# Optimization experiments

Measured on AMD Instinct MI355X. Metric: run time of the kernel, lower is better.

Reference implementation:

```python
import jax, jax.numpy as jnp
import numpy as np

B, T = 64, 512
V, D, H = 50000, 256, 256  # vocab, word-embed dim, LSTM hidden


def _lstm_dir(x, Wih, Whh, bih, bhh):
    """Unidirectional LSTM over time (PyTorch gate order i,f,g,o). x: [B,T,D_in] -> [B,T,H]."""
    xp = jnp.einsum('btd,gd->btg', x, Wih) + bih + bhh  # precompute input projections [B,T,4H]
    xp = xp.transpose(1, 0, 2)  # [T,B,4H]
    Hh = Whh.shape[1]
    h0 = jnp.zeros((x.shape[0], Hh), x.dtype)

    def step(carry, xt):
        h, c = carry
        g = xt + h @ Whh.T
        i, f, gg, o = jnp.split(g, 4, axis=-1)
        c = jax.nn.sigmoid(f) * c + jax.nn.sigmoid(i) * jnp.tanh(gg)
        h = jax.nn.sigmoid(o) * jnp.tanh(c)
        return (h, c), h

    _, hs = jax.lax.scan(step, (h0, h0), xp)
    return hs.transpose(1, 0, 2)  # [B,T,H]


def _bidir(x, rev_idx, pf, pb):
    """Length-aware bidirectional layer: reverse only the valid prefix (emulates pack_padded_sequence)."""
    hf = _lstm_dir(x, *pf)
    xr = jnp.take_along_axis(x, rev_idx[..., None], axis=1)   # reversed valid prefix
    hb = _lstm_dir(xr, *pb)
    hb = jnp.take_along_axis(hb, rev_idx[..., None], axis=1)  # flip back (involution on valid part)
    return jnp.concatenate([hf, hb], axis=-1)  # [B,T,2H]


def setup_inputs() -> dict:
    key = jax.random.key(0)
    ks = jax.random.split(key, 24)
    x = jax.random.randint(ks[0], (B, T), 0, V - 1)          # avoid padding_idx = V-1
    sentlen = jax.random.randint(ks[1], (B,), 1, T + 1)       # ragged lengths in [1, T]
    embed = (jax.random.normal(ks[2], (V, D), jnp.float32) * 0.1).at[V - 1].set(0.0)
    inp = {"x": x, "sentlen": sentlen, "embed": embed}
    k = 3
    for layer, in_dim in [(0, D), (1, 2 * H)]:
        for d in ["f", "b"]:
            s = 1.0 / np.sqrt(H)
            inp[f"Wih{layer}{d}"] = jax.random.uniform(ks[k], (4 * H, in_dim), jnp.float32, -s, s); k += 1
            inp[f"Whh{layer}{d}"] = jax.random.uniform(ks[k], (4 * H, H), jnp.float32, -s, s); k += 1
            inp[f"bih{layer}{d}"] = jax.random.uniform(ks[k], (4 * H,), jnp.float32, -s, s); k += 1
            inp[f"bhh{layer}{d}"] = jax.random.uniform(ks[k], (4 * H,), jnp.float32, -s, s); k += 1
    return inp


def reference(x, sentlen, embed,
              Wih0f, Whh0f, bih0f, bhh0f, Wih0b, Whh0b, bih0b, bhh0b,
              Wih1f, Whh1f, bih1f, bhh1f, Wih1b, Whh1b, bih1b, bhh1b):
    emb = embed[x]  # [B,T,D]; dropout is a no-op in eval mode
    t = jnp.arange(x.shape[1])
    valid = t[None, :] < sentlen[:, None]                       # [B,T]
    rev_idx = jnp.where(valid, sentlen[:, None] - 1 - t[None, :], t[None, :])
    h1 = _bidir(emb, rev_idx, (Wih0f, Whh0f, bih0f, bhh0f), (Wih0b, Whh0b, bih0b, bhh0b))
    h2 = _bidir(h1, rev_idx, (Wih1f, Whh1f, bih1f, bhh1f), (Wih1b, Whh1b, bih1b, bhh1b))
    # ragged max-pool over valid positions (replaces the per-sample Python loop)
    feat = jnp.max(jnp.where(valid[..., None], h2, -jnp.inf), axis=1)  # [B,2H]
    return feat[None]  # [1,B,2H]
```

## Files before the change

### kernel.cpp

```cpp
#include <hip/hip_runtime.h>
#include <stdint.h>
#include <stddef.h>

#define BATCH 64
#define TT    512
#define DIM   256
#define HID   256
#define MROWS (BATCH*TT)

typedef unsigned short u16;
typedef unsigned int u32;
typedef __attribute__((ext_vector_type(8))) short  short8;
typedef __attribute__((ext_vector_type(4))) float  f32x4;
typedef __attribute__((ext_vector_type(4))) int    int4v;
typedef __attribute__((ext_vector_type(4))) unsigned short u16x4;

__device__ __forceinline__ u16 bf16_hi(float f) {
    union { float f; unsigned u; } v; v.f = f;
    unsigned r = v.u + 0x7fffu + ((v.u >> 16) & 1u);
    return (u16)(r >> 16);
}
__device__ __forceinline__ float bf16f(u16 b) {
    union { unsigned u; float f; } v; v.u = ((unsigned)b) << 16;
    return v.f;
}
__device__ __forceinline__ float fsigmoid(float x) { return 1.f / (1.f + __expf(-x)); }
__device__ __forceinline__ float ftanh(float x) {
    x = fminf(15.f, fmaxf(-15.f, x));
    float e = __expf(2.f * x);
    return (e - 1.f) / (e + 1.f);
}

__global__ __launch_bounds__(256) void k_prep(
    const float* __restrict__ Wih0f, const float* __restrict__ Whh0f, const float* __restrict__ bih0f, const float* __restrict__ bhh0f,
    const float* __restrict__ Wih0b, const float* __restrict__ Whh0b, const float* __restrict__ bih0b, const float* __restrict__ bhh0b,
    const float* __restrict__ Wih1f, const float* __restrict__ Whh1f, const float* __restrict__ bih1f, const float* __restrict__ bhh1f,
    const float* __restrict__ Wih1b, const float* __restrict__ Whh1b, const float* __restrict__ bih1b, const float* __restrict__ bhh1b,
    u16* __restrict__ WihQ0hi, u16* __restrict__ WihQ0lo,
    u16* __restrict__ WhhQ0hi, u16* __restrict__ WhhQ0lo,
    u16* __restrict__ WihQ1hi, u16* __restrict__ WihQ1lo,
    u16* __restrict__ WhhQ1hi, u16* __restrict__ WhhQ1lo,
    float* __restrict__ bsum, u32* __restrict__ hxp)
{
    const int i = blockIdx.x * 256 + threadIdx.x;
    if (i < 2621440) {
        const float* src; u16* dhi; u16* dlo; int off;
        if      (i <  262144) { src = Wih0f; dhi = WihQ0hi;          dlo = WihQ0lo;          off = i; }
        else if (i <  524288) { src = Wih0b; dhi = WihQ0hi + 262144; dlo = WihQ0lo + 262144; off = i -  262144; }
        else if (i <  786432) { src = Whh0f; dhi = WhhQ0hi;          dlo = WhhQ0lo;          off = i -  524288; }
        else if (i < 1048576) { src = Whh0b; dhi = WhhQ0hi + 262144; dlo = WhhQ0lo + 262144; off = i -  786432; }
        else if (i < 1572864) { src = Wih1f; dhi = WihQ1hi;          dlo = WihQ1lo;          off = i - 1048576; }
        else if (i < 2097152) { src = Wih1b; dhi = WihQ1hi + 524288; dlo = WihQ1lo + 524288; off = i - 1572864; }
        else if (i < 2359296) { src = Whh1f; dhi = WhhQ1hi;          dlo = WhhQ1lo;          off = i - 2097152; }
        else                  { src = Whh1b; dhi = WhhQ1hi + 262144; dlo = WhhQ1lo + 262144; off = i - 2359296; }
        const float v = src[off];
        const u16 h = bf16_hi(v);
        dhi[off] = h;
        dlo[off] = bf16_hi(v - bf16f(h));
    } else if (i < 2621440 + 4096) {
        const int j = i - 2621440;
        const float* bihs[4] = { bih0f, bih0b, bih1f, bih1b };
        const float* bhhs[4] = { bhh0f, bhh0b, bhh1f, bhh1b };
        const int ld = j >> 10, k = j & 1023;
        bsum[j] = bihs[ld][k] + bhhs[ld][k];
    } else if (i < 2621440 + 4096 + 131072) {
        const int j = i - (2621440 + 4096);
        hxp[j] = ((j >> 15) & 1) ? 0x00010000u : 0u;
    }
}

__global__ __launch_bounds__(256) void k_gather(
    const int* __restrict__ x, const float* __restrict__ embed, u16* __restrict__ A0)
{
    const int row = blockIdx.x * 4 + (threadIdx.x >> 6);
    const int col = (threadIdx.x & 63) * 4;
    const int xi = x[row];
    const f32x4 v = *(const f32x4*)(embed + (size_t)xi * DIM + col);
    u16x4 h;
    #pragma unroll
    for (int i = 0; i < 4; i++) h[i] = bf16_hi(v[i]);
    *(u16x4*)(A0 + (size_t)row * DIM + col) = h;
}

template<int KIN, bool WRITE_H, bool POOL>
__global__ __launch_bounds__(256, 1) void k_lstm(
    const u16* __restrict__ Xin,
    const u16* __restrict__ WhhHi, const u16* __restrict__ WhhLo,
    const u16* __restrict__ WihHi, const u16* __restrict__ WihLo,
    const float* __restrict__ bsum,
    const int* __restrict__ slen,
    u16* __restrict__ H0,
    float* __restrict__ outp,
    u32* __restrict__ hx)
{
    constexpr int KV = KIN / 32;
    constexpr int CR = KIN / 8;
    constexpr int NST = (16 * CR) / 256;

    const int bid = blockIdx.x;
    const int s = bid >> 3;
    const int d = (bid >> 2) & 1;
    const int c = bid & 3;
    const int tid = threadIdx.x;
    const int l = tid & 63, w = tid >> 6;

    __shared__ u16 xs[16 * KIN];
    __shared__ u16 hs_hi[16 * 256];
    __shared__ u16 hs_lo[16 * 256];
    __shared__ float g_lds[64 * 16];
    __shared__ u32 ho_pack[16 * 16];
    __shared__ int lens_sh[16];
    __shared__ int maxlen_sh;

    if (tid < 16) lens_sh[tid] = slen[c * 16 + tid];
    __syncthreads();
    if (tid == 0) {
        int m = 0;
        #pragma unroll
        for (int i = 0; i < 16; i++) m = max(m, lens_sh[i]);
        maxlen_sh = m;
    }
    __syncthreads();
    const int maxlen = maxlen_sh;

    const int rbase = d * 1024 + w * 256 + s * 16;
    short8 wfh[8], wfl[8];
    #pragma unroll
    for (int kv = 0; kv < 8; kv++) {
        const size_t off = (size_t)(rbase + (l & 15)) * 256 + kv * 32 + ((l >> 4) << 3);
        wfh[kv] = *(const short8*)(WhhHi + off);
        wfl[kv] = *(const short8*)(WhhLo + off);
    }
    short8 uih[KV], uil[KV];
    #pragma unroll
    for (int kv = 0; kv < KV; kv++) {
        const size_t off = (size_t)(rbase + (l & 15)) * KIN + kv * 32 + ((l >> 4) << 3);
        uih[kv] = *(const short8*)(WihHi + off);
        uil[kv] = *(const short8*)(WihLo + off);
    }
    #pragma unroll
    for (int kv = 0; kv < 8; kv++) {
        asm volatile("" : "+v"(wfh[kv]), "+v"(wfl[kv]));
    }
    #pragma unroll
    for (int kv = 0; kv < KV; kv++) {
        asm volatile("" : "+v"(uih[kv]), "+v"(uil[kv]));
    }
    float bias_g[4];
    {
        const int u = tid >> 4;
        #pragma unroll
        for (int g = 0; g < 4; g++) bias_g[g] = bsum[d * 1024 + g * 256 + s * 16 + u];
    }

    float creg = 0.f, mx = -1e30f;
    const int bi_m = l & 15;
    const int swz = bi_m & 7;
    const int klane = l >> 4;

    for (int t = 0; t < maxlen; ++t) {
        #pragma unroll
        for (int p = 0; p < NST; p++) {
            const int idx = p * 256 + tid;
            const int bi = idx / CR;
            const int ch = idx % CR;
            const int len_b = lens_sh[bi];
            const int pos = (d == 0) ? t : ((t < len_b) ? (len_b - 1 - t) : t);
            const short8 v = *(const short8*)(Xin + ((size_t)(c * 16 + bi) * TT + pos) * KIN + ch * 8);
            *(short8*)(xs + bi * KIN + (ch ^ (bi & 7)) * 8) = v;
        }

        if (t == 0) {
            const short8 z = {0,0,0,0,0,0,0,0};
            for (int i = tid; i < 512; i += 256) {
                ((short8*)hs_hi)[i] = z;
                ((short8*)hs_lo)[i] = z;
            }
        } else {
            const u32* gbase = hx + (((size_t)(t & 1) * 2 + d) * 64 + c * 16) * 256;
            const u32* p0 = gbase + tid * 4;
            const u32* p1 = p0 + 1024;
            const u32* p2 = p0 + 2048;
            const u32* p3 = p0 + 3072;
            const int expect = (t >> 1) & 1;
            int4v w0, w1, w2, w3;
            int rounds = 0;
            for (;;) {
                asm volatile(
                    "global_load_dwordx4 %0, %4, off sc0 sc1\n\t"
                    "global_load_dwordx4 %1, %5, off sc0 sc1\n\t"
                    "global_load_dwordx4 %2, %6, off sc0 sc1\n\t"
                    "global_load_dwordx4 %3, %7, off sc0 sc1"
                    : "=&v"(w0), "=&v"(w1), "=&v"(w2), "=&v"(w3)
                    : "v"(p0), "v"(p1), "v"(p2), "v"(p3)
                    : "memory");
                asm volatile("s_waitcnt vmcnt(0)"
                    : "+v"(w0), "+v"(w1), "+v"(w2), "+v"(w3) :: "memory");
                u32 aw = 0xFFFFFFFFu, ow = 0u;
                #pragma unroll
                for (int j = 0; j < 4; j++) {
                    aw &= (u32)w0[j]; ow |= (u32)w0[j];
                    aw &= (u32)w1[j]; ow |= (u32)w1[j];
                    aw &= (u32)w2[j]; ow |= (u32)w2[j];
                    aw &= (u32)w3[j]; ow |= (u32)w3[j];
                }
                const int ok = expect ? (int)((aw >> 16) & 1u)
                                      : (int)(((ow >> 16) & 1u) ^ 1u);
                if (__all(ok)) break;
                if (++rounds > (1 << 17)) break;
                __builtin_amdgcn_s_sleep(1);
            }
            const int u0 = (tid & 63) * 4;
            const int ch = u0 >> 3;
            const int co = u0 & 7;
            int4v wq[4] = {w0, w1, w2, w3};
            #pragma unroll
            for (int q = 0; q < 4; q++) {
                const int bi = q * 4 + (tid >> 6);
                u16x4 hi4, lo4;
                #pragma unroll
                for (int j = 0; j < 4; j++) {
                    const u32 wd = (u32)wq[q][j];
                    hi4[j] = (u16)(wd & 0xFFFFu);
                    lo4[j] = (u16)(wd >> 16);
                }
                *(u16x4*)(hs_hi + bi * 256 + (ch ^ (bi & 7)) * 8 + co) = hi4;
                *(u16x4*)(hs_lo + bi * 256 + (ch ^ (bi & 7)) * 8 + co) = lo4;
            }
        }
        __syncthreads();

        f32x4 acc_a = {0.f,0.f,0.f,0.f}, acc_b = {0.f,0.f,0.f,0.f}, acc_c = {0.f,0.f,0.f,0.f};
        #pragma unroll
        for (int kv = 0; kv < 8; kv++) {
            const int kc = kv * 4 + klane;
            const short8 bh = *(const short8*)(hs_hi + bi_m * 256 + (kc ^ swz) * 8);
            const short8 bl = *(const short8*)(hs_lo + bi_m * 256 + (kc ^ swz) * 8);
            acc_a = __builtin_amdgcn_mfma_f32_16x16x32_bf16(wfh[kv], bh, acc_a, 0, 0, 0);
            acc_b = __builtin_amdgcn_mfma_f32_16x16x32_bf16(wfl[kv], bh, acc_b, 0, 0, 0);
            acc_c = __builtin_amdgcn_mfma_f32_16x16x32_bf16(wfh[kv], bl, acc_c, 0, 0, 0);
        }
        #pragma unroll
        for (int kv = 0; kv < KV; kv++) {
            const int kc = kv * 4 + klane;
            const short8 bx = *(const short8*)(xs + bi_m * KIN + (kc ^ swz) * 8);
            acc_a = __builtin_amdgcn_mfma_f32_16x16x32_bf16(uih[kv], bx, acc_a, 0, 0, 0);
            acc_b = __builtin_amdgcn_mfma_f32_16x16x32_bf16(uil[kv], bx, acc_b, 0, 0, 0);
        }
        {
            const int r0 = w * 16 + klane * 4;
            #pragma unroll
            for (int r = 0; r < 4; r++)
                g_lds[(r0 + r) * 16 + bi_m] = (acc_a[r] + acc_b[r]) + acc_c[r];
        }
        __syncthreads();

        {
            const int u = tid >> 4, bi = tid & 15;
            const float gi = g_lds[( 0 + u) * 16 + bi] + bias_g[0];
            const float gf = g_lds[(16 + u) * 16 + bi] + bias_g[1];
            const float gg = g_lds[(32 + u) * 16 + bi] + bias_g[2];
            const float go = g_lds[(48 + u) * 16 + bi] + bias_g[3];
            const float cc = fsigmoid(gf) * creg + fsigmoid(gi) * ftanh(gg);
            creg = cc;
            const float h = fsigmoid(go) * ftanh(cc);
            if (POOL && t < lens_sh[bi]) mx = fmaxf(mx, h);
            const u16 hh = bf16_hi(h);
            const u32 hl = ((u32)bf16_hi(h - bf16f(hh)) & 0xFFFEu) | (u32)(((t + 1) >> 1) & 1);
            ho_pack[bi * 16 + u] = (u32)hh | (hl << 16);
        }
        __syncthreads();

        if (w == 0) {
            const int bi = l >> 2, q = l & 3;
            const int4v pv = *(const int4v*)(ho_pack + bi * 16 + q * 4);
            u32* dst = hx + (((size_t)((t + 1) & 1) * 2 + d) * 64 + c * 16 + bi) * 256 + s * 16 + q * 4;
            asm volatile("global_store_dwordx4 %0, %1, off sc0 sc1" :: "v"(dst), "v"(pv) : "memory");
        } else if (WRITE_H && w == 1) {
            const int bi = l >> 2, q = l & 3;
            const int4v pv = *(const int4v*)(ho_pack + bi * 16 + q * 4);
            u16x4 hv;
            #pragma unroll
            for (int j = 0; j < 4; j++) hv[j] = (u16)((u32)pv[j] & 0xFFFFu);
            const int len_b = lens_sh[bi];
            const int pos = (d == 0) ? t : ((t < len_b) ? (len_b - 1 - t) : t);
            *(u16x4*)(H0 + ((size_t)(c * 16 + bi) * TT + pos) * 512 + d * 256 + s * 16 + q * 4) = hv;
        }
    }

    if (POOL) {
        const int u = tid >> 4, bi = tid & 15;
        outp[(size_t)(c * 16 + bi) * 512 + d * 256 + s * 16 + u] = mx;
    }
}

extern "C" void kernel_launch(void* const* d_in, const int* in_sizes, int n_in,
                              void* d_out, int out_size, void* d_ws, size_t ws_size,
                              hipStream_t stream)
{
    (void)in_sizes; (void)n_in; (void)out_size; (void)ws_size;
    const int*   x     = (const int*)d_in[0];
    const int*   slen  = (const int*)d_in[1];
    const float* embed = (const float*)d_in[2];
    const float* W[16];
    for (int i = 0; i < 16; i++) W[i] = (const float*)d_in[3 + i];
    float* out = (float*)d_out;

    char* p = (char*)d_ws;
    u16* A0      = (u16*)p;   p += (size_t)MROWS * DIM * 2;
    u16* H0      = (u16*)p;   p += (size_t)MROWS * 512 * 2;
    u16* WihQ0hi = (u16*)p;   p += 524288 * 2;
    u16* WihQ0lo = (u16*)p;   p += 524288 * 2;
    u16* WhhQ0hi = (u16*)p;   p += 524288 * 2;
    u16* WhhQ0lo = (u16*)p;   p += 524288 * 2;
    u16* WihQ1hi = (u16*)p;   p += 1048576 * 2;
    u16* WihQ1lo = (u16*)p;   p += 1048576 * 2;
    u16* WhhQ1hi = (u16*)p;   p += 524288 * 2;
    u16* WhhQ1lo = (u16*)p;   p += 524288 * 2;
    float* bsum  = (float*)p; p += 4096 * 4;
    u32* hxp     = (u32*)p;   p += 131072 * 4;

    k_prep<<<10768, 256, 0, stream>>>(
        W[0], W[1], W[2], W[3], W[4], W[5], W[6], W[7],
        W[8], W[9], W[10], W[11], W[12], W[13], W[14], W[15],
        WihQ0hi, WihQ0lo, WhhQ0hi, WhhQ0lo, WihQ1hi, WihQ1lo, WhhQ1hi, WhhQ1lo,
        bsum, hxp);

    k_gather<<<8192, 256, 0, stream>>>(x, embed, A0);

    k_lstm<256, true, false><<<128, 256, 0, stream>>>(
        A0, WhhQ0hi, WhhQ0lo, WihQ0hi, WihQ0lo, bsum, slen,
        H0, nullptr, hxp);

    k_lstm<512, false, true><<<128, 256, 0, stream>>>(
        H0, WhhQ1hi, WhhQ1lo, WihQ1hi, WihQ1lo, bsum + 2048, slen,
        nullptr, out, hxp + 65536);
}
```

Measured before the change: 2.603 ms.

## Permute weight rows so each lane holds all four gates, dropping gate LDS exchange

```diff
diff --git a/kernel.cpp b/kernel.cpp
--- a/kernel.cpp
+++ b/kernel.cpp
@@ -44,16 +44,21 @@
 {
     const int i = blockIdx.x * 256 + threadIdx.x;
     if (i < 2621440) {
-        const float* src; u16* dhi; u16* dlo; int off;
-        if      (i <  262144) { src = Wih0f; dhi = WihQ0hi;          dlo = WihQ0lo;          off = i; }
-        else if (i <  524288) { src = Wih0b; dhi = WihQ0hi + 262144; dlo = WihQ0lo + 262144; off = i -  262144; }
-        else if (i <  786432) { src = Whh0f; dhi = WhhQ0hi;          dlo = WhhQ0lo;          off = i -  524288; }
-        else if (i < 1048576) { src = Whh0b; dhi = WhhQ0hi + 262144; dlo = WhhQ0lo + 262144; off = i -  786432; }
-        else if (i < 1572864) { src = Wih1f; dhi = WihQ1hi;          dlo = WihQ1lo;          off = i - 1048576; }
-        else if (i < 2097152) { src = Wih1b; dhi = WihQ1hi + 524288; dlo = WihQ1lo + 524288; off = i - 1572864; }
-        else if (i < 2359296) { src = Whh1f; dhi = WhhQ1hi;          dlo = WhhQ1lo;          off = i - 2097152; }
-        else                  { src = Whh1b; dhi = WhhQ1hi + 262144; dlo = WhhQ1lo + 262144; off = i - 2359296; }
-        const float v = src[off];
+        const float* srcf; const float* srcb; u16* dhi; u16* dlo; int off; int K;
+        if      (i <  524288) { srcf = Wih0f; srcb = Wih0b; dhi = WihQ0hi; dlo = WihQ0lo; off = i;           K = 256; }
+        else if (i < 1048576) { srcf = Whh0f; srcb = Whh0b; dhi = WhhQ0hi; dlo = WhhQ0lo; off = i -  524288; K = 256; }
+        else if (i < 2097152) { srcf = Wih1f; srcb = Wih1b; dhi = WihQ1hi; dlo = WihQ1lo; off = i - 1048576; K = 512; }
+        else                  { srcf = Whh1f; srcb = Whh1b; dhi = WhhQ1hi; dlo = WhhQ1lo; off = i - 2097152; K = 256; }
+        const int SZ = 1024 * K;
+        const int dd = off / SZ;
+        const int o  = off - dd * SZ;
+        const int pr = o / K;
+        const int k  = o - pr * K;
+        const int s  = pr >> 6;
+        const int ww = (pr >> 4) & 3;
+        const int m  = pr & 15;
+        const int src_row = (m & 3) * 256 + s * 16 + ww * 4 + (m >> 2);
+        const float v = (dd ? srcb : srcf)[src_row * K + k];
         const u16 h = bf16_hi(v);
         dhi[off] = h;
         dlo[off] = bf16_hi(v - bf16f(h));
@@ -107,8 +112,7 @@
     __shared__ u16 xs[16 * KIN];
     __shared__ u16 hs_hi[16 * 256];
     __shared__ u16 hs_lo[16 * 256];
-    __shared__ float g_lds[64 * 16];
-    __shared__ u32 ho_pack[16 * 16];
+    __shared__ u32 ho_pack[16 * 17];
     __shared__ int lens_sh[16];
     __shared__ int maxlen_sh;
 
@@ -123,51 +127,49 @@
     __syncthreads();
     const int maxlen = maxlen_sh;
 
-    const int rbase = d * 1024 + w * 256 + s * 16;
+    const int wblk = (d * 16 + s) * 4 + w;
     short8 wfh[8], wfl[8];
     #pragma unroll
     for (int kv = 0; kv < 8; kv++) {
-        const size_t off = (size_t)(rbase + (l & 15)) * 256 + kv * 32 + ((l >> 4) << 3);
+        const size_t off = (size_t)(wblk * 16 + (l & 15)) * 256 + kv * 32 + ((l >> 4) << 3);
         wfh[kv] = *(const short8*)(WhhHi + off);
         wfl[kv] = *(const short8*)(WhhLo + off);
     }
     short8 uih[KV], uil[KV];
     #pragma unroll
     for (int kv = 0; kv < KV; kv++) {
-        const size_t off = (size_t)(rbase + (l & 15)) * KIN + kv * 32 + ((l >> 4) << 3);
+        const size_t off = (size_t)(wblk * 16 + (l & 15)) * KIN + kv * 32 + ((l >> 4) << 3);
         uih[kv] = *(const short8*)(WihHi + off);
         uil[kv] = *(const short8*)(WihLo + off);
     }
     #pragma unroll
-    for (int kv = 0; kv < 8; kv++) {
-        asm volatile("" : "+v"(wfh[kv]), "+v"(wfl[kv]));
-    }
-    #pragma unroll
-    for (int kv = 0; kv < KV; kv++) {
-        asm volatile("" : "+v"(uih[kv]), "+v"(uil[kv]));
-    }
+    for (int kv = 0; kv < 8; kv++) asm volatile("" : "+v"(wfh[kv]), "+v"(wfl[kv]));
+    #pragma unroll
+    for (int kv = 0; kv < KV; kv++) asm volatile("" : "+v"(uih[kv]), "+v"(uil[kv]));
+
+    const int q_u  = l >> 4;
+    const int bi_m = l & 15;
+    const int unit = s * 16 + w * 4 + q_u;
     float bias_g[4];
-    {
-        const int u = tid >> 4;
-        #pragma unroll
-        for (int g = 0; g < 4; g++) bias_g[g] = bsum[d * 1024 + g * 256 + s * 16 + u];
-    }
+    #pragma unroll
+    for (int g = 0; g < 4; g++) bias_g[g] = bsum[d * 1024 + g * 256 + unit];
 
     float creg = 0.f, mx = -1e30f;
-    const int bi_m = l & 15;
     const int swz = bi_m & 7;
     const int klane = l >> 4;
+    const int len_m = lens_sh[bi_m];
 
     for (int t = 0; t < maxlen; ++t) {
+        short8 xreg[NST];
         #pragma unroll
         for (int p = 0; p < NST; p++) {
             const int idx = p * 256 + tid;
             const int bi = idx / CR;
-            const int ch = idx % CR;
+            const int ch = idx - bi * CR;
             const int len_b = lens_sh[bi];
             const int pos = (d == 0) ? t : ((t < len_b) ? (len_b - 1 - t) : t);
-            const short8 v = *(const short8*)(Xin + ((size_t)(c * 16 + bi) * TT + pos) * KIN + ch * 8);
-            *(short8*)(xs + bi * KIN + (ch ^ (bi & 7)) * 8) = v;
+            xreg[p] = *(const short8*)(Xin + ((size_t)(c * 16 + bi) * TT + pos) * KIN + ch * 8);
+            asm volatile("" : "+v"(xreg[p]));
         }
 
         if (t == 0) {
@@ -215,18 +217,25 @@
             const int co = u0 & 7;
             int4v wq[4] = {w0, w1, w2, w3};
             #pragma unroll
-            for (int q = 0; q < 4; q++) {
-                const int bi = q * 4 + (tid >> 6);
+            for (int qq = 0; qq < 4; qq++) {
+                const int bi = qq * 4 + (tid >> 6);
                 u16x4 hi4, lo4;
                 #pragma unroll
                 for (int j = 0; j < 4; j++) {
-                    const u32 wd = (u32)wq[q][j];
+                    const u32 wd = (u32)wq[qq][j];
                     hi4[j] = (u16)(wd & 0xFFFFu);
                     lo4[j] = (u16)(wd >> 16);
                 }
                 *(u16x4*)(hs_hi + bi * 256 + (ch ^ (bi & 7)) * 8 + co) = hi4;
                 *(u16x4*)(hs_lo + bi * 256 + (ch ^ (bi & 7)) * 8 + co) = lo4;
             }
+        }
+        #pragma unroll
+        for (int p = 0; p < NST; p++) {
+            const int idx = p * 256 + tid;
+            const int bi = idx / CR;
+            const int ch = idx - bi * CR;
+            *(short8*)(xs + bi * KIN + (ch ^ (bi & 7)) * 8) = xreg[p];
         }
         __syncthreads();
 
@@ -247,50 +256,41 @@
             acc_a = __builtin_amdgcn_mfma_f32_16x16x32_bf16(uih[kv], bx, acc_a, 0, 0, 0);
             acc_b = __builtin_amdgcn_mfma_f32_16x16x32_bf16(uil[kv], bx, acc_b, 0, 0, 0);
         }
+
         {
-            const int r0 = w * 16 + klane * 4;
-            #pragma unroll
-            for (int r = 0; r < 4; r++)
-                g_lds[(r0 + r) * 16 + bi_m] = (acc_a[r] + acc_b[r]) + acc_c[r];
-        }
-        __syncthreads();
-
-        {
-            const int u = tid >> 4, bi = tid & 15;
-            const float gi = g_lds[( 0 + u) * 16 + bi] + bias_g[0];
-            const float gf = g_lds[(16 + u) * 16 + bi] + bias_g[1];
-            const float gg = g_lds[(32 + u) * 16 + bi] + bias_g[2];
-            const float go = g_lds[(48 + u) * 16 + bi] + bias_g[3];
+            const float gi = acc_a[0] + acc_b[0] + acc_c[0] + bias_g[0];
+            const float gf = acc_a[1] + acc_b[1] + acc_c[1] + bias_g[1];
+            const float gg = acc_a[2] + acc_b[2] + acc_c[2] + bias_g[2];
+            const float go = acc_a[3] + acc_b[3] + acc_c[3] + bias_g[3];
             const float cc = fsigmoid(gf) * creg + fsigmoid(gi) * ftanh(gg);
             creg = cc;
             const float h = fsigmoid(go) * ftanh(cc);
-            if (POOL && t < lens_sh[bi]) mx = fmaxf(mx, h);
+            if (POOL && t < len_m) mx = fmaxf(mx, h);
             const u16 hh = bf16_hi(h);
             const u32 hl = ((u32)bf16_hi(h - bf16f(hh)) & 0xFFFEu) | (u32)(((t + 1) >> 1) & 1);
-            ho_pack[bi * 16 + u] = (u32)hh | (hl << 16);
+            ho_pack[bi_m * 17 + w * 4 + q_u] = (u32)hh | (hl << 16);
         }
         __syncthreads();
 
         if (w == 0) {
-            const int bi = l >> 2, q = l & 3;
-            const int4v pv = *(const int4v*)(ho_pack + bi * 16 + q * 4);
-            u32* dst = hx + (((size_t)((t + 1) & 1) * 2 + d) * 64 + c * 16 + bi) * 256 + s * 16 + q * 4;
+            const int bi = l >> 2, qq = l & 3;
+            const int4v pv = *(const int4v*)(ho_pack + bi * 17 + qq * 4);
+            u32* dst = hx + (((size_t)((t + 1) & 1) * 2 + d) * 64 + c * 16 + bi) * 256 + s * 16 + qq * 4;
             asm volatile("global_store_dwordx4 %0, %1, off sc0 sc1" :: "v"(dst), "v"(pv) : "memory");
         } else if (WRITE_H && w == 1) {
-            const int bi = l >> 2, q = l & 3;
-            const int4v pv = *(const int4v*)(ho_pack + bi * 16 + q * 4);
+            const int bi = l >> 2, qq = l & 3;
+            const int4v pv = *(const int4v*)(ho_pack + bi * 17 + qq * 4);
             u16x4 hv;
             #pragma unroll
             for (int j = 0; j < 4; j++) hv[j] = (u16)((u32)pv[j] & 0xFFFFu);
             const int len_b = lens_sh[bi];
             const int pos = (d == 0) ? t : ((t < len_b) ? (len_b - 1 - t) : t);
-            *(u16x4*)(H0 + ((size_t)(c * 16 + bi) * TT + pos) * 512 + d * 256 + s * 16 + q * 4) = hv;
+            *(u16x4*)(H0 + ((size_t)(c * 16 + bi) * TT + pos) * 512 + d * 256 + s * 16 + qq * 4) = hv;
         }
     }
 
     if (POOL) {
-        const int u = tid >> 4, bi = tid & 15;
-        outp[(size_t)(c * 16 + bi) * 512 + d * 256 + s * 16 + u] = mx;
+        outp[(size_t)(c * 16 + bi_m) * 512 + d * 256 + unit] = mx;
     }
 }
 
```

Result: slower. 2.673 ms (+2.7%).
